# Optimization experiments

Measured on AMD Instinct MI355X. Metric: run time of the kernel, lower is better.

Reference implementation:

```python
import jax, jax.numpy as jnp
import numpy as np

N_NODES = 100000


def _gcn_norm(edge_src, edge_dst, n):
    ones = jnp.ones(edge_src.shape[0], dtype=jnp.float32)
    deg_out = jax.ops.segment_sum(ones, edge_src, num_segments=n)
    deg_in = jax.ops.segment_sum(ones, edge_dst, num_segments=n)
    norm_src = jax.lax.rsqrt(jnp.maximum(deg_out, 1.0))
    norm_dst = jax.lax.rsqrt(jnp.maximum(deg_in, 1.0))
    return norm_src, norm_dst


def _graph_conv(h, edge_src, edge_dst, norm_src, norm_dst, W, b, act):
    # symmetric-normalized aggregation: D^-1/2 A D^-1/2 h, then linear
    m = (h * norm_src[:, None])[edge_src]                       # [E, d] gather
    agg = jax.ops.segment_sum(m, edge_dst, num_segments=h.shape[0])  # [N, d] scatter-add
    agg = agg * norm_dst[:, None]
    out = agg @ W + b[: W.shape[1]]
    return act(out) if act is not None else out


def setup_inputs() -> dict:
    key = jax.random.key(0)
    ks = jax.random.split(key, 8)
    d_in, d_h, n_cls, E = 64, 64, 40, 1000000
    return {
        "features": jax.random.normal(ks[0], (N_NODES, d_in), dtype=jnp.float32),
        "edge_src": jax.random.randint(ks[1], (E,), 0, N_NODES),
        "edge_dst": jax.random.randint(ks[2], (E,), 0, N_NODES),
        "W1": jax.random.normal(ks[3], (d_in, d_h), dtype=jnp.float32) * (1.0 / np.sqrt(d_in)),
        "b1": jnp.zeros((d_h,), dtype=jnp.float32),
        "W2": jax.random.normal(ks[4], (d_h, d_h), dtype=jnp.float32) * (1.0 / np.sqrt(d_h)),
        "b2": jnp.zeros((d_h,), dtype=jnp.float32),
        "W3": jax.random.normal(ks[5], (d_h, n_cls), dtype=jnp.float32) * (1.0 / np.sqrt(d_h)),
        "b3": jnp.zeros((d_h,), dtype=jnp.float32),
    }


def reference(features, edge_src, edge_dst, W1, b1, W2, b2, W3, b3):
    norm_src, norm_dst = _gcn_norm(edge_src, edge_dst, features.shape[0])
    h = _graph_conv(features, edge_src, edge_dst, norm_src, norm_dst, W1, b1, jax.nn.relu)
    h = _graph_conv(h, edge_src, edge_dst, norm_src, norm_dst, W2, b2, jax.nn.relu)
    h = _graph_conv(h, edge_src, edge_dst, norm_src, norm_dst, W3, b3, None)
    return h
```

## Files before the change

kernel.cpp:

```cpp
#include <hip/hip_runtime.h>

#define D 64
#define THREADS 256
#define CAP 40

__global__ void build_kernel(const int* __restrict__ src, const int* __restrict__ dst,
                             int* __restrict__ cnt_out, int* __restrict__ cursor,
                             int* __restrict__ eidx, int E) {
    int i = blockIdx.x * blockDim.x + threadIdx.x;
    if (i < E) {
        int s = src[i];
        int d = dst[i];
        atomicAdd(&cnt_out[s], 1);
        int pos = atomicAdd(&cursor[d], 1);
        if (pos < CAP) eidx[(size_t)d * CAP + pos] = s;
    }
}

__global__ void prescale_kernel(const float* __restrict__ feat, const int* __restrict__ cnt_out,
                                float* __restrict__ outp, int n16) {
    int i = blockIdx.x * blockDim.x + threadIdx.x;
    if (i < n16) {
        float s = rsqrtf(fmaxf((float)cnt_out[i >> 4], 1.0f));
        float4 v = ((const float4*)feat)[i];
        v.x *= s; v.y *= s; v.z *= s; v.w *= s;
        ((float4*)outp)[i] = v;
    }
}

__device__ __forceinline__ float bcast(float v, int l) {
    return __uint_as_float(__builtin_amdgcn_readlane(__float_as_uint(v), l));
}

template <int DOUT, bool RELU, bool SOUT>
__global__ __launch_bounds__(THREADS)
void layer_kernel(const float* __restrict__ h, const int* __restrict__ deg,
                  const int* __restrict__ eidx, const int* __restrict__ cnt_out,
                  const float* __restrict__ W, const float* __restrict__ b,
                  float* __restrict__ out, int n) {
    const int t = threadIdx.x;
    const int wave = t >> 6;
    const int lane = t & 63;
    const int grp  = lane >> 4;
    const int c    = lane & 15;
    const int ln   = (lane < DOUT) ? lane : (DOUT - 1);

    float4 Wc[16];
#pragma unroll
    for (int k4 = 0; k4 < 16; ++k4) {
        Wc[k4].x = W[(4 * k4 + 0) * DOUT + ln];
        Wc[k4].y = W[(4 * k4 + 1) * DOUT + ln];
        Wc[k4].z = W[(4 * k4 + 2) * DOUT + ln];
        Wc[k4].w = W[(4 * k4 + 3) * DOUT + ln];
    }
    const float bl = b[ln];

    const int nquads = (n + 3) >> 2;
    for (int qd = blockIdx.x * 4 + wave; qd < nquads; qd += gridDim.x * 4) {
        int node0 = qd * 4;
        int node  = node0 + grp;
        bool valid = node < n;
        int node_c = valid ? node : 0;
        int dg = valid ? deg[node_c] : 0;
        if (dg > CAP) dg = CAP;
        size_t start = (size_t)node_c * CAP;

        float4 a0 = {0.f, 0.f, 0.f, 0.f};
        float4 a1 = {0.f, 0.f, 0.f, 0.f};
        for (int e = 0; e < dg; e += 4) {
            int4 i4 = *(const int4*)(eidx + start + e);
            int rem = dg - e;
            unsigned s0 = (unsigned)i4.x;
            unsigned s1 = (rem > 1) ? (unsigned)i4.y : 0u;
            unsigned s2 = (rem > 2) ? (unsigned)i4.z : 0u;
            unsigned s3 = (rem > 3) ? (unsigned)i4.w : 0u;
            float w1 = (rem > 1) ? 1.f : 0.f;
            float w2 = (rem > 2) ? 1.f : 0.f;
            float w3 = (rem > 3) ? 1.f : 0.f;
            float4 v0 = *((const float4*)(h + ((size_t)s0 << 6)) + c);
            float4 v1 = *((const float4*)(h + ((size_t)s1 << 6)) + c);
            float4 v2 = *((const float4*)(h + ((size_t)s2 << 6)) + c);
            float4 v3 = *((const float4*)(h + ((size_t)s3 << 6)) + c);
            a0.x += v0.x; a0.y += v0.y; a0.z += v0.z; a0.w += v0.w;
            a0.x = fmaf(v1.x, w1, a0.x); a0.y = fmaf(v1.y, w1, a0.y);
            a0.z = fmaf(v1.z, w1, a0.z); a0.w = fmaf(v1.w, w1, a0.w);
            a1.x = fmaf(v2.x, w2, a1.x); a1.y = fmaf(v2.y, w2, a1.y);
            a1.z = fmaf(v2.z, w2, a1.z); a1.w = fmaf(v2.w, w2, a1.w);
            a1.x = fmaf(v3.x, w3, a1.x); a1.y = fmaf(v3.y, w3, a1.y);
            a1.z = fmaf(v3.z, w3, a1.z); a1.w = fmaf(v3.w, w3, a1.w);
        }
        float ax = a0.x + a1.x, ay = a0.y + a1.y;
        float az = a0.z + a1.z, aw = a0.w + a1.w;

        float sA = 0.f, sB = 0.f, sC = 0.f, sD = 0.f;
#pragma unroll
        for (int cc = 0; cc < 16; ++cc) {
            sA = fmaf(bcast(ax,      cc), Wc[cc].x, sA);
            sB = fmaf(bcast(ax, 16 + cc), Wc[cc].x, sB);
            sC = fmaf(bcast(ax, 32 + cc), Wc[cc].x, sC);
            sD = fmaf(bcast(ax, 48 + cc), Wc[cc].x, sD);
            sA = fmaf(bcast(ay,      cc), Wc[cc].y, sA);
            sB = fmaf(bcast(ay, 16 + cc), Wc[cc].y, sB);
            sC = fmaf(bcast(ay, 32 + cc), Wc[cc].y, sC);
            sD = fmaf(bcast(ay, 48 + cc), Wc[cc].y, sD);
            sA = fmaf(bcast(az,      cc), Wc[cc].z, sA);
            sB = fmaf(bcast(az, 16 + cc), Wc[cc].z, sB);
            sC = fmaf(bcast(az, 32 + cc), Wc[cc].z, sC);
            sD = fmaf(bcast(az, 48 + cc), Wc[cc].z, sD);
            sA = fmaf(bcast(aw,      cc), Wc[cc].w, sA);
            sB = fmaf(bcast(aw, 16 + cc), Wc[cc].w, sB);
            sC = fmaf(bcast(aw, 32 + cc), Wc[cc].w, sC);
            sD = fmaf(bcast(aw, 48 + cc), Wc[cc].w, sD);
        }

        int dg0 = __builtin_amdgcn_readlane(dg, 0);
        int dg1 = __builtin_amdgcn_readlane(dg, 16);
        int dg2 = __builtin_amdgcn_readlane(dg, 32);
        int dg3 = __builtin_amdgcn_readlane(dg, 48);
        float nd0 = rsqrtf(fmaxf((float)dg0, 1.f));
        float nd1 = rsqrtf(fmaxf((float)dg1, 1.f));
        float nd2 = rsqrtf(fmaxf((float)dg2, 1.f));
        float nd3 = rsqrtf(fmaxf((float)dg3, 1.f));
        float ns0 = 1.f, ns1 = 1.f, ns2 = 1.f, ns3 = 1.f;
        if (SOUT) {
            ns0 = rsqrtf(fmaxf((float)cnt_out[node0], 1.f));
            ns1 = (node0 + 1 < n) ? rsqrtf(fmaxf((float)cnt_out[node0 + 1], 1.f)) : 0.f;
            ns2 = (node0 + 2 < n) ? rsqrtf(fmaxf((float)cnt_out[node0 + 2], 1.f)) : 0.f;
            ns3 = (node0 + 3 < n) ? rsqrtf(fmaxf((float)cnt_out[node0 + 3], 1.f)) : 0.f;
        }

        float o0 = fmaf(sA, nd0, bl);
        float o1 = fmaf(sB, nd1, bl);
        float o2 = fmaf(sC, nd2, bl);
        float o3 = fmaf(sD, nd3, bl);
        if (RELU) {
            o0 = fmaxf(o0, 0.f); o1 = fmaxf(o1, 0.f);
            o2 = fmaxf(o2, 0.f); o3 = fmaxf(o3, 0.f);
        }
        if (SOUT) { o0 *= ns0; o1 *= ns1; o2 *= ns2; o3 *= ns3; }
        if (lane < DOUT) {
            out[(size_t)node0 * DOUT + lane] = o0;
            if (node0 + 1 < n) out[(size_t)(node0 + 1) * DOUT + lane] = o1;
            if (node0 + 2 < n) out[(size_t)(node0 + 2) * DOUT + lane] = o2;
            if (node0 + 3 < n) out[(size_t)(node0 + 3) * DOUT + lane] = o3;
        }
    }
}

extern "C" void kernel_launch(void* const* d_in, const int* in_sizes, int n_in,
                              void* d_out, int out_size, void* d_ws, size_t ws_size,
                              hipStream_t stream) {
    const float* feat = (const float*)d_in[0];
    const int*   esrc = (const int*)d_in[1];
    const int*   edst = (const int*)d_in[2];
    const float* W1   = (const float*)d_in[3];
    const float* b1   = (const float*)d_in[4];
    const float* W2   = (const float*)d_in[5];
    const float* b2   = (const float*)d_in[6];
    const float* W3   = (const float*)d_in[7];
    const float* b3   = (const float*)d_in[8];
    float* out = (float*)d_out;

    const int E = in_sizes[1];
    const int N = in_sizes[0] / D;

    int* cnt_out = (int*)d_ws;
    int* cursor  = cnt_out + N;
    int* eidx    = cursor + N;
    float* hA    = (float*)(eidx + (size_t)N * CAP);
    float* hB    = hA + (size_t)N * D;

    hipMemsetAsync(cnt_out, 0, (size_t)2 * N * sizeof(int), stream);

    const int eblocks = (E + THREADS - 1) / THREADS;
    build_kernel<<<eblocks, THREADS, 0, stream>>>(esrc, edst, cnt_out, cursor, eidx, E);

    const int n16 = N * (D / 4);
    prescale_kernel<<<(n16 + THREADS - 1) / THREADS, THREADS, 0, stream>>>(feat, cnt_out, hB, n16);

    const int lgrid = 2048;
    layer_kernel<D, true, true><<<lgrid, THREADS, 0, stream>>>(
        hB, cursor, eidx, cnt_out, W1, b1, hA, N);
    layer_kernel<D, true, true><<<lgrid, THREADS, 0, stream>>>(
        hA, cursor, eidx, cnt_out, W2, b2, hB, N);
    layer_kernel<40, false, false><<<lgrid, THREADS, 0, stream>>>(
        hB, cursor, eidx, cnt_out, W3, b3, out, N);
}
```

Before: 382.1 us.

## Store intermediate node features in fp16 and vectorize edge build loads

```diff
diff --git a/kernel.cpp b/kernel.cpp
--- a/kernel.cpp
+++ b/kernel.cpp
@@ -1,4 +1,5 @@
 #include <hip/hip_runtime.h>
+#include <hip/hip_fp16.h>
 
 #define D 64
 #define THREADS 256
@@ -7,24 +8,44 @@
 __global__ void build_kernel(const int* __restrict__ src, const int* __restrict__ dst,
                              int* __restrict__ cnt_out, int* __restrict__ cursor,
                              int* __restrict__ eidx, int E) {
-    int i = blockIdx.x * blockDim.x + threadIdx.x;
-    if (i < E) {
-        int s = src[i];
-        int d = dst[i];
-        atomicAdd(&cnt_out[s], 1);
-        int pos = atomicAdd(&cursor[d], 1);
-        if (pos < CAP) eidx[(size_t)d * CAP + pos] = s;
+    int base = (blockIdx.x * blockDim.x + threadIdx.x) * 4;
+    if (base + 3 < E) {
+        int4 s4 = *(const int4*)(src + base);
+        int4 d4 = *(const int4*)(dst + base);
+        atomicAdd(&cnt_out[s4.x], 1);
+        atomicAdd(&cnt_out[s4.y], 1);
+        atomicAdd(&cnt_out[s4.z], 1);
+        atomicAdd(&cnt_out[s4.w], 1);
+        int p0 = atomicAdd(&cursor[d4.x], 1);
+        int p1 = atomicAdd(&cursor[d4.y], 1);
+        int p2 = atomicAdd(&cursor[d4.z], 1);
+        int p3 = atomicAdd(&cursor[d4.w], 1);
+        if (p0 < CAP) eidx[(size_t)d4.x * CAP + p0] = s4.x;
+        if (p1 < CAP) eidx[(size_t)d4.y * CAP + p1] = s4.y;
+        if (p2 < CAP) eidx[(size_t)d4.z * CAP + p2] = s4.z;
+        if (p3 < CAP) eidx[(size_t)d4.w * CAP + p3] = s4.w;
+    } else {
+        for (int i = base; i < E; ++i) {
+            int s = src[i], d = dst[i];
+            atomicAdd(&cnt_out[s], 1);
+            int pos = atomicAdd(&cursor[d], 1);
+            if (pos < CAP) eidx[(size_t)d * CAP + pos] = s;
+        }
     }
 }
 
 __global__ void prescale_kernel(const float* __restrict__ feat, const int* __restrict__ cnt_out,
-                                float* __restrict__ outp, int n16) {
+                                __half* __restrict__ outp, int n16) {
     int i = blockIdx.x * blockDim.x + threadIdx.x;
     if (i < n16) {
         float s = rsqrtf(fmaxf((float)cnt_out[i >> 4], 1.0f));
         float4 v = ((const float4*)feat)[i];
-        v.x *= s; v.y *= s; v.z *= s; v.w *= s;
-        ((float4*)outp)[i] = v;
+        __half2 lo = __floats2half2_rn(v.x * s, v.y * s);
+        __half2 hi = __floats2half2_rn(v.z * s, v.w * s);
+        uint2 u;
+        u.x = *(unsigned*)&lo;
+        u.y = *(unsigned*)&hi;
+        ((uint2*)outp)[i] = u;
     }
 }
 
@@ -32,12 +53,12 @@
     return __uint_as_float(__builtin_amdgcn_readlane(__float_as_uint(v), l));
 }
 
-template <int DOUT, bool RELU, bool SOUT>
+template <int DOUT, bool RELU, bool SOUT, bool OUT_HALF>
 __global__ __launch_bounds__(THREADS)
-void layer_kernel(const float* __restrict__ h, const int* __restrict__ deg,
+void layer_kernel(const __half* __restrict__ h, const int* __restrict__ deg,
                   const int* __restrict__ eidx, const int* __restrict__ cnt_out,
                   const float* __restrict__ W, const float* __restrict__ b,
-                  float* __restrict__ out, int n) {
+                  void* __restrict__ outv, int n) {
     const int t = threadIdx.x;
     const int wave = t >> 6;
     const int lane = t & 63;
@@ -65,8 +86,8 @@
         if (dg > CAP) dg = CAP;
         size_t start = (size_t)node_c * CAP;
 
-        float4 a0 = {0.f, 0.f, 0.f, 0.f};
-        float4 a1 = {0.f, 0.f, 0.f, 0.f};
+        float ax = 0.f, ay = 0.f, az = 0.f, aw = 0.f;
+        float bx = 0.f, by = 0.f, bz = 0.f, bw = 0.f;
         for (int e = 0; e < dg; e += 4) {
             int4 i4 = *(const int4*)(eidx + start + e);
             int rem = dg - e;
@@ -77,20 +98,23 @@
             float w1 = (rem > 1) ? 1.f : 0.f;
             float w2 = (rem > 2) ? 1.f : 0.f;
             float w3 = (rem > 3) ? 1.f : 0.f;
-            float4 v0 = *((const float4*)(h + ((size_t)s0 << 6)) + c);
-            float4 v1 = *((const float4*)(h + ((size_t)s1 << 6)) + c);
-            float4 v2 = *((const float4*)(h + ((size_t)s2 << 6)) + c);
-            float4 v3 = *((const float4*)(h + ((size_t)s3 << 6)) + c);
-            a0.x += v0.x; a0.y += v0.y; a0.z += v0.z; a0.w += v0.w;
-            a0.x = fmaf(v1.x, w1, a0.x); a0.y = fmaf(v1.y, w1, a0.y);
-            a0.z = fmaf(v1.z, w1, a0.z); a0.w = fmaf(v1.w, w1, a0.w);
-            a1.x = fmaf(v2.x, w2, a1.x); a1.y = fmaf(v2.y, w2, a1.y);
-            a1.z = fmaf(v2.z, w2, a1.z); a1.w = fmaf(v2.w, w2, a1.w);
-            a1.x = fmaf(v3.x, w3, a1.x); a1.y = fmaf(v3.y, w3, a1.y);
-            a1.z = fmaf(v3.z, w3, a1.z); a1.w = fmaf(v3.w, w3, a1.w);
-        }
-        float ax = a0.x + a1.x, ay = a0.y + a1.y;
-        float az = a0.z + a1.z, aw = a0.w + a1.w;
+            uint2 u0 = *((const uint2*)(h + ((size_t)s0 << 6)) + c);
+            uint2 u1 = *((const uint2*)(h + ((size_t)s1 << 6)) + c);
+            uint2 u2 = *((const uint2*)(h + ((size_t)s2 << 6)) + c);
+            uint2 u3 = *((const uint2*)(h + ((size_t)s3 << 6)) + c);
+            float2 l0 = __half22float2(*(__half2*)&u0.x), h0 = __half22float2(*(__half2*)&u0.y);
+            float2 l1 = __half22float2(*(__half2*)&u1.x), h1 = __half22float2(*(__half2*)&u1.y);
+            float2 l2 = __half22float2(*(__half2*)&u2.x), h2 = __half22float2(*(__half2*)&u2.y);
+            float2 l3 = __half22float2(*(__half2*)&u3.x), h3 = __half22float2(*(__half2*)&u3.y);
+            ax += l0.x; ay += l0.y; az += h0.x; aw += h0.y;
+            ax = fmaf(l1.x, w1, ax); ay = fmaf(l1.y, w1, ay);
+            az = fmaf(h1.x, w1, az); aw = fmaf(h1.y, w1, aw);
+            bx = fmaf(l2.x, w2, bx); by = fmaf(l2.y, w2, by);
+            bz = fmaf(h2.x, w2, bz); bw = fmaf(h2.y, w2, bw);
+            bx = fmaf(l3.x, w3, bx); by = fmaf(l3.y, w3, by);
+            bz = fmaf(h3.x, w3, bz); bw = fmaf(h3.y, w3, bw);
+        }
+        ax += bx; ay += by; az += bz; aw += bw;
 
         float sA = 0.f, sB = 0.f, sC = 0.f, sD = 0.f;
 #pragma unroll
@@ -139,10 +163,19 @@
         }
         if (SOUT) { o0 *= ns0; o1 *= ns1; o2 *= ns2; o3 *= ns3; }
         if (lane < DOUT) {
-            out[(size_t)node0 * DOUT + lane] = o0;
-            if (node0 + 1 < n) out[(size_t)(node0 + 1) * DOUT + lane] = o1;
-            if (node0 + 2 < n) out[(size_t)(node0 + 2) * DOUT + lane] = o2;
-            if (node0 + 3 < n) out[(size_t)(node0 + 3) * DOUT + lane] = o3;
+            if (OUT_HALF) {
+                __half* out = (__half*)outv;
+                out[(size_t)node0 * DOUT + lane] = __float2half(o0);
+                if (node0 + 1 < n) out[(size_t)(node0 + 1) * DOUT + lane] = __float2half(o1);
+                if (node0 + 2 < n) out[(size_t)(node0 + 2) * DOUT + lane] = __float2half(o2);
+                if (node0 + 3 < n) out[(size_t)(node0 + 3) * DOUT + lane] = __float2half(o3);
+            } else {
+                float* out = (float*)outv;
+                out[(size_t)node0 * DOUT + lane] = o0;
+                if (node0 + 1 < n) out[(size_t)(node0 + 1) * DOUT + lane] = o1;
+                if (node0 + 2 < n) out[(size_t)(node0 + 2) * DOUT + lane] = o2;
+                if (node0 + 3 < n) out[(size_t)(node0 + 3) * DOUT + lane] = o3;
+            }
         }
     }
 }
@@ -167,22 +200,23 @@
     int* cnt_out = (int*)d_ws;
     int* cursor  = cnt_out + N;
     int* eidx    = cursor + N;
-    float* hA    = (float*)(eidx + (size_t)N * CAP);
-    float* hB    = hA + (size_t)N * D;
+    __half* hA   = (__half*)(eidx + (size_t)N * CAP);
+    __half* hB   = hA + (size_t)N * D;
 
     hipMemsetAsync(cnt_out, 0, (size_t)2 * N * sizeof(int), stream);
 
-    const int eblocks = (E + THREADS - 1) / THREADS;
-    build_kernel<<<eblocks, THREADS, 0, stream>>>(esrc, edst, cnt_out, cursor, eidx, E);
+    const int ethreads4 = (E + 3) / 4;
+    build_kernel<<<(ethreads4 + THREADS - 1) / THREADS, THREADS, 0, stream>>>(
+        esrc, edst, cnt_out, cursor, eidx, E);
 
     const int n16 = N * (D / 4);
     prescale_kernel<<<(n16 + THREADS - 1) / THREADS, THREADS, 0, stream>>>(feat, cnt_out, hB, n16);
 
     const int lgrid = 2048;
-    layer_kernel<D, true, true><<<lgrid, THREADS, 0, stream>>>(
+    layer_kernel<D, true, true, true><<<lgrid, THREADS, 0, stream>>>(
         hB, cursor, eidx, cnt_out, W1, b1, hA, N);
-    layer_kernel<D, true, true><<<lgrid, THREADS, 0, stream>>>(
+    layer_kernel<D, true, true, true><<<lgrid, THREADS, 0, stream>>>(
         hA, cursor, eidx, cnt_out, W2, b2, hB, N);
-    layer_kernel<40, false, false><<<lgrid, THREADS, 0, stream>>>(
+    layer_kernel<40, false, false, false><<<lgrid, THREADS, 0, stream>>>(
         hB, cursor, eidx, cnt_out, W3, b3, out, N);
 }
```

After: 378.8 us. Within noise of the previous version (-0.9%).
